# Kernel tuning notes

Hardware: AMD Instinct MI355X
Metric: run time of the kernel (lower is better)

Reference implementation:

```python
import jax, jax.numpy as jnp
import numpy as np

N = 50000
EPS = 1e-16


def _gat_conv(x, w, att_src, att_dst, bias, src, dst, heads, out_ch, concat):
    # x: [N, F_in]; w: [heads*out_ch, F_in]; att_*: [heads, out_ch]; bias: [heads*out_ch] or [out_ch]
    n = x.shape[0]
    xw = (x @ w.T).reshape(n, heads, out_ch)              # [N, H, C]
    a_src = jnp.einsum('nhc,hc->nh', xw, att_src)          # [N, H]
    a_dst = jnp.einsum('nhc,hc->nh', xw, att_dst)
    alpha = a_src[src] + a_dst[dst]                        # [E, H]
    alpha = jax.nn.leaky_relu(alpha, negative_slope=0.2)
    # segment softmax over destination node (every node has a self loop)
    m = jax.ops.segment_max(alpha, dst, num_segments=n)    # [N, H]
    e = jnp.exp(alpha - m[dst])
    s = jax.ops.segment_sum(e, dst, num_segments=n)        # [N, H]
    coef = e / (s[dst] + EPS)                              # [E, H]
    out = jax.ops.segment_sum(xw[src] * coef[:, :, None], dst, num_segments=n)  # [N, H, C]
    if concat:
        out = out.reshape(n, heads * out_ch)
    else:
        out = out.mean(axis=1)
    return out + bias


def setup_inputs() -> dict:
    key = jax.random.key(0)
    ks = jax.random.split(key, 8)
    F_in, H, C1, NC = 128, 2, 64, 16
    E = 1_600_000
    x = jax.random.normal(ks[0], (N, F_in), dtype=jnp.float32)
    edge_index = jax.random.randint(ks[1], (2, E), 0, N, dtype=jnp.int64)
    w1 = jax.random.normal(ks[2], (H * C1, F_in), dtype=jnp.float32) / np.sqrt(F_in)
    att_src1 = jax.random.normal(ks[3], (H, C1), dtype=jnp.float32) / np.sqrt(C1)
    att_dst1 = jax.random.normal(ks[4], (H, C1), dtype=jnp.float32) / np.sqrt(C1)
    b1 = jnp.zeros((H * C1,), dtype=jnp.float32)
    w2 = jax.random.normal(ks[5], (NC, H * C1), dtype=jnp.float32) / np.sqrt(H * C1)
    att_src2 = jax.random.normal(ks[6], (1, NC), dtype=jnp.float32) / np.sqrt(NC)
    att_dst2 = jax.random.normal(ks[7], (1, NC), dtype=jnp.float32) / np.sqrt(NC)
    b2 = jnp.zeros((NC,), dtype=jnp.float32)
    return {"x": x, "edge_index": edge_index, "w1": w1, "att_src1": att_src1,
            "att_dst1": att_dst1, "b1": b1, "w2": w2, "att_src2": att_src2,
            "att_dst2": att_dst2, "b2": b2}


def reference(x, edge_index, w1, att_src1, att_dst1, b1, w2, att_src2, att_dst2, b2):
    n = x.shape[0]
    loop = jnp.arange(n, dtype=edge_index.dtype)
    src = jnp.concatenate([edge_index[0], loop])  # PyG adds self loops by default
    dst = jnp.concatenate([edge_index[1], loop])
    h = _gat_conv(x, w1, att_src1, att_dst1, b1, src, dst, heads=2, out_ch=64, concat=True)
    h = jax.nn.relu(h)
    # dropout p=0.5 is identity in eval mode
    out = _gat_conv(h, w2, att_src2, att_dst2, b2, src, dst, heads=1, out_ch=16, concat=True)
    return out
```

## Files before the change

kernel.cpp:

```cpp
#include <hip/hip_runtime.h>
#include <hip/hip_fp16.h>


#define BSHIFT 7
#define MAXB 512

using f16x8 = __attribute__((ext_vector_type(8))) _Float16;
using f16x4 = __attribute__((ext_vector_type(4))) _Float16;
using f32x4 = __attribute__((ext_vector_type(4))) float;

__device__ __forceinline__ float lrelu(float a) { return fmaxf(a, 0.2f * a); }


__global__ __launch_bounds__(256) void init_cursor_kernel(int* __restrict__ bincur,
                                                          int B, int CAP) {
  int i = blockIdx.x * 256 + threadIdx.x;
  if (i < B) bincur[i] = i * CAP;
}

__global__ __launch_bounds__(256) void partition_kernel(const int* __restrict__ src,
                                                        const int* __restrict__ dst,
                                                        int* __restrict__ bincur,
                                                        unsigned* __restrict__ binned,
                                                        int E, int B, int CH) {
  __shared__ int s_h[MAXB];
  __shared__ int s_base[MAXB];
  __shared__ int s_cur[MAXB];
  for (int i = threadIdx.x; i < B; i += 256) s_h[i] = 0;
  __syncthreads();
  int lo = blockIdx.x * CH, hi = min(lo + CH, E);
  for (int e = lo + threadIdx.x; e < hi; e += 256)
    atomicAdd(&s_h[dst[e] >> BSHIFT], 1);
  __syncthreads();
  for (int i = threadIdx.x; i < B; i += 256) {
    int c = s_h[i];
    s_base[i] = c ? atomicAdd(&bincur[i], c) : 0;
    s_cur[i] = 0;
  }
  __syncthreads();
  for (int e = lo + threadIdx.x; e < hi; e += 256) {
    int d = dst[e];
    int b = d >> BSHIFT;
    int r = atomicAdd(&s_cur[b], 1);
    binned[s_base[b] + r] = (unsigned)src[e] | ((unsigned)(d & 127) << 16);
  }
}

__global__ __launch_bounds__(256) void bucket_build_kernel(const unsigned* __restrict__ binned,
                                                           const int* __restrict__ bincur,
                                                           int2* __restrict__ nodeseg,
                                                           int* __restrict__ csr,
                                                           int N, int CAP) {
  __shared__ int s_deg[128];
  __shared__ int s_cur[128];
  __shared__ int s_wsum;
  int b = blockIdx.x;
  int lo = b * CAP, hi = bincur[b];
  int t = threadIdx.x;
  if (t < 128) s_deg[t] = 0;
  __syncthreads();
  for (int i = lo + t; i < hi; i += 256)
    atomicAdd(&s_deg[binned[i] >> 16], 1);
  __syncthreads();
  int lane = t & 63, wv = t >> 6;
  int v = (t < 128) ? s_deg[t] : 0;
  int incl = v;
#pragma unroll
  for (int off = 1; off < 64; off <<= 1) {
    int u = __shfl_up(incl, off);
    if (lane >= off) incl += u;
  }
  if (t == 63) s_wsum = incl;
  __syncthreads();
  int excl = incl - v + ((wv == 1) ? s_wsum : 0);
  if (t < 128) {
    int node = (b << BSHIFT) + t;
    if (node < N) nodeseg[node] = make_int2(lo + excl, lo + excl + v);
    s_cur[t] = lo + excl;
  }
  __syncthreads();
  for (int i = lo + t; i < hi; i += 256) {
    unsigned e = binned[i];
    int p = atomicAdd(&s_cur[e >> 16], 1);
    csr[p] = (int)(e & 0xFFFFu);
  }
}


#define XS 136
__global__ __launch_bounds__(256) void gemm1_kernel(const float* __restrict__ x,
                                                    const float* __restrict__ w1,
                                                    const float* __restrict__ as1,
                                                    const float* __restrict__ ad1,
                                                    __half* __restrict__ xw1h,
                                                    float* __restrict__ asrc1,
                                                    float* __restrict__ adst1, int N) {
  __shared__ __align__(16) _Float16 lx[64 * XS];
  __shared__ __align__(16) _Float16 lw[128 * XS];
  int t = threadIdx.x;
  int n0 = blockIdx.x * 64;

#pragma unroll
  for (int j = 0; j < 8; ++j) {
    int idx = t + 256 * j;
    int nd = idx >> 5, i4 = (idx & 31) * 4;
    int gn = n0 + nd;
    float4 v = (gn < N) ? *(const float4*)&x[(size_t)gn * 128 + i4]
                        : make_float4(0.f, 0.f, 0.f, 0.f);
    f16x4 h;
    h[0] = (_Float16)v.x; h[1] = (_Float16)v.y;
    h[2] = (_Float16)v.z; h[3] = (_Float16)v.w;
    *(f16x4*)&lx[nd * XS + i4] = h;
  }
#pragma unroll
  for (int j = 0; j < 16; ++j) {
    int idx = t + 256 * j;
    int o = idx >> 5, i4 = (idx & 31) * 4;
    float4 v = *(const float4*)&w1[(size_t)o * 128 + i4];
    f16x4 h;
    h[0] = (_Float16)v.x; h[1] = (_Float16)v.y;
    h[2] = (_Float16)v.z; h[3] = (_Float16)v.w;
    *(f16x4*)&lw[o * XS + i4] = h;
  }
  __syncthreads();

  int lane = t & 63, wv = t >> 6;
  int m16 = lane & 15, q = lane >> 4;

  f32x4 acc[8];
#pragma unroll
  for (int i = 0; i < 8; ++i) acc[i] = (f32x4){0.f, 0.f, 0.f, 0.f};

#pragma unroll
  for (int c = 0; c < 4; ++c) {
    f16x8 a = *(const f16x8*)&lx[(16 * wv + m16) * XS + c * 32 + q * 8];
#pragma unroll
    for (int tt = 0; tt < 8; ++tt) {
      f16x8 b = *(const f16x8*)&lw[(tt * 16 + m16) * XS + c * 32 + q * 8];
      acc[tt] = __builtin_amdgcn_mfma_f32_16x16x32_f16(a, b, acc[tt], 0, 0, 0);
    }
  }

#pragma unroll
  for (int tt = 0; tt < 8; ++tt) {
#pragma unroll
    for (int r = 0; r < 4; ++r) {
      lx[(16 * wv + 4 * q + r) * XS + tt * 16 + m16] = (_Float16)acc[tt][r];
    }
  }

  {
    float ps = 0.f, pd = 0.f;
    int p = q;
#pragma unroll
    for (int k = 0; k < 4; ++k) {
      f16x8 hv = *(const f16x8*)&lx[(16 * wv + m16) * XS + p * 32 + k * 8];
      float4 s0 = *(const float4*)&as1[p * 32 + k * 8];
      float4 s1 = *(const float4*)&as1[p * 32 + k * 8 + 4];
      float4 d0 = *(const float4*)&ad1[p * 32 + k * 8];
      float4 d1 = *(const float4*)&ad1[p * 32 + k * 8 + 4];
      ps += (float)hv[0] * s0.x + (float)hv[1] * s0.y + (float)hv[2] * s0.z +
            (float)hv[3] * s0.w + (float)hv[4] * s1.x + (float)hv[5] * s1.y +
            (float)hv[6] * s1.z + (float)hv[7] * s1.w;
      pd += (float)hv[0] * d0.x + (float)hv[1] * d0.y + (float)hv[2] * d0.z +
            (float)hv[3] * d0.w + (float)hv[4] * d1.x + (float)hv[5] * d1.y +
            (float)hv[6] * d1.z + (float)hv[7] * d1.w;
    }
    ps += __shfl_xor(ps, 16);
    pd += __shfl_xor(pd, 16);
    int n = n0 + 16 * wv + m16;
    if (n < N && (q == 0 || q == 2)) {
      int hh = q >> 1;
      asrc1[2 * n + hh] = ps;
      adst1[2 * n + hh] = pd;
    }
  }

#pragma unroll
  for (int i = 0; i < 4; ++i) {
    int m = q + 4 * i;
    int n = n0 + 16 * wv + m;
    if (n < N) {
      uint4 v = *(const uint4*)&lx[(16 * wv + m) * XS + m16 * 8];
      *(uint4*)&xw1h[(size_t)n * 128 + m16 * 8] = v;
    }
  }
}

__global__ __launch_bounds__(256) void agg1_kernel(const __half* __restrict__ xw1h,
                                                   const float* __restrict__ asrc1,
                                                   const float* __restrict__ adst1,
                                                   const float* __restrict__ b1,
                                                   const float* __restrict__ w2,
                                                   const float* __restrict__ as2,
                                                   const float* __restrict__ ad2,
                                                   const int* __restrict__ csr,
                                                   const int2* __restrict__ nodeseg,
                                                   __half* __restrict__ xw2h,
                                                   float* __restrict__ asrc2,
                                                   float* __restrict__ adst2, int N) {
  __shared__ int s_off[4][64];
  __shared__ float2 s_w[4][64];
  int lane = threadIdx.x & 63, wv = threadIdx.x >> 6;
  int d = blockIdx.x * 4 + wv;
  if (d >= N) return;
  int c8 = lane & 15;
  int row = lane >> 4;
  int head = c8 >> 3;
  int2 seg = nodeseg[d];
  int e0 = seg.x, e1 = seg.y;
  float2 asv = *(const float2*)&asrc1[2 * d];
  float2 adv = *(const float2*)&adst1[2 * d];
  float wself = __expf(lrelu(head ? (asv.y + adv.y) : (asv.x + adv.x)));

  const char* xb = (const char*)xw1h + 16 * c8;

  float a[8];
  float sum = 0.f;
#pragma unroll
  for (int k = 0; k < 8; ++k) a[k] = 0.f;
  if (row == 0) {
    uint4 r = *(const uint4*)(xb + ((size_t)d << 8));
    const __half2* hp = (const __half2*)&r;
#pragma unroll
    for (int k = 0; k < 4; ++k) {
      float2 v = __half22float2(hp[k]);
      a[2 * k] = wself * v.x;
      a[2 * k + 1] = wself * v.y;
    }
    sum = wself;
  }

  for (int base = e0; base < e1; base += 64) {
    int cnt = min(64, e1 - base);
    if (lane < cnt) {
      int s = csr[base + lane];
      float2 aa = *(const float2*)&asrc1[2 * s];
      s_off[wv][lane] = s << 8;
      float2 w;
      w.x = __expf(lrelu(aa.x + adv.x));
      w.y = __expf(lrelu(aa.y + adv.y));
      s_w[wv][lane] = w;
    }
    int j = 0;
    for (; j + 7 < cnt; j += 8) {
      int oA = s_off[wv][j + row];
      int oB = s_off[wv][j + 4 + row];
      float wA = ((const float*)&s_w[wv][j + row])[head];
      float wB = ((const float*)&s_w[wv][j + 4 + row])[head];
      uint4 rA = *(const uint4*)(xb + oA);
      uint4 rB = *(const uint4*)(xb + oB);
      const __half2* hA = (const __half2*)&rA;
      const __half2* hB = (const __half2*)&rB;
#pragma unroll
      for (int k = 0; k < 4; ++k) {
        float2 vA = __half22float2(hA[k]);
        float2 vB = __half22float2(hB[k]);
        a[2 * k] += wA * vA.x + wB * vB.x;
        a[2 * k + 1] += wA * vA.y + wB * vB.y;
      }
      sum += wA + wB;
    }
    for (; j < cnt; j += 4) {
      if (row < cnt - j) {
        int oA = s_off[wv][j + row];
        float wA = ((const float*)&s_w[wv][j + row])[head];
        uint4 rA = *(const uint4*)(xb + oA);
        const __half2* hA = (const __half2*)&rA;
#pragma unroll
        for (int k = 0; k < 4; ++k) {
          float2 vA = __half22float2(hA[k]);
          a[2 * k] += wA * vA.x;
          a[2 * k + 1] += wA * vA.y;
        }
        sum += wA;
      }
    }
  }

#pragma unroll
  for (int k = 0; k < 8; ++k) {
    a[k] += __shfl_xor(a[k], 16);
    a[k] += __shfl_xor(a[k], 32);
  }
  sum += __shfl_xor(sum, 16);
  sum += __shfl_xor(sum, 32);

  float inv = 1.f / (sum + 1e-16f);
  float4 blo = *(const float4*)&b1[8 * c8];
  float4 bhi = *(const float4*)&b1[8 * c8 + 4];
  float h[8];
  h[0] = fmaxf(a[0] * inv + blo.x, 0.f);
  h[1] = fmaxf(a[1] * inv + blo.y, 0.f);
  h[2] = fmaxf(a[2] * inv + blo.z, 0.f);
  h[3] = fmaxf(a[3] * inv + blo.w, 0.f);
  h[4] = fmaxf(a[4] * inv + bhi.x, 0.f);
  h[5] = fmaxf(a[5] * inv + bhi.y, 0.f);
  h[6] = fmaxf(a[6] * inv + bhi.z, 0.f);
  h[7] = fmaxf(a[7] * inv + bhi.w, 0.f);

  float p[4];
#pragma unroll
  for (int cc = 0; cc < 4; ++cc) {
    const float4 wlo = *(const float4*)&w2[(row * 4 + cc) * 128 + 8 * c8];
    const float4 whi = *(const float4*)&w2[(row * 4 + cc) * 128 + 8 * c8 + 4];
    p[cc] = h[0] * wlo.x + h[1] * wlo.y + h[2] * wlo.z + h[3] * wlo.w +
            h[4] * whi.x + h[5] * whi.y + h[6] * whi.z + h[7] * whi.w;
#pragma unroll
    for (int k = 1; k < 16; k <<= 1) p[cc] += __shfl_xor(p[cc], k);
  }
  float qs = 0.f, qd = 0.f;
#pragma unroll
  for (int cc = 0; cc < 4; ++cc) {
    qs += p[cc] * as2[row * 4 + cc];
    qd += p[cc] * ad2[row * 4 + cc];
  }
  qs += __shfl_xor(qs, 16);
  qs += __shfl_xor(qs, 32);
  qd += __shfl_xor(qd, 16);
  qd += __shfl_xor(qd, 32);
  if (lane == 0) {
    asrc2[d] = qs;
    adst2[d] = qd;
  }
  if (c8 == 0) {
    union {
      __half hh[4];
      uint2 u;
    } pk;
#pragma unroll
    for (int cc = 0; cc < 4; ++cc) pk.hh[cc] = __float2half(p[cc]);
    *(uint2*)&xw2h[(size_t)d * 16 + row * 4] = pk.u;
  }
}

__global__ __launch_bounds__(256) void agg2_kernel(const __half* __restrict__ xw2h,
                                                   const float* __restrict__ asrc2,
                                                   const float* __restrict__ adst2,
                                                   const float* __restrict__ b2,
                                                   const int* __restrict__ csr,
                                                   const int2* __restrict__ nodeseg,
                                                   float* __restrict__ out, int N) {
  __shared__ int s_off[4][64];
  __shared__ float s_w[4][64];
  int lane = threadIdx.x & 63, wv = threadIdx.x >> 6;
  int d = blockIdx.x * 4 + wv;
  if (d >= N) return;
  int c2 = lane & 7;
  int row = lane >> 3;
  int2 seg = nodeseg[d];
  int e0 = seg.x, e1 = seg.y;
  float advd = adst2[d];
  float wself = __expf(lrelu(asrc2[d] + advd));
  const char* xb = (const char*)xw2h + 4 * c2;

  float a0 = 0.f, a1 = 0.f, sum = 0.f;
  if (row == 0) {
    float2 v = __half22float2(*(const __half2*)(xb + (size_t)d * 32));
    a0 = wself * v.x;
    a1 = wself * v.y;
    sum = wself;
  }
  for (int base = e0; base < e1; base += 64) {
    int cnt = min(64, e1 - base);
    if (lane < cnt) {
      int s = csr[base + lane];
      s_off[wv][lane] = s << 5;
      s_w[wv][lane] = __expf(lrelu(asrc2[s] + advd));
    }
    int j = 0;
    for (; j + 15 < cnt; j += 16) {
      int o0 = s_off[wv][j + row];
      int o1 = s_off[wv][j + 8 + row];
      float w0 = s_w[wv][j + row];
      float w1 = s_w[wv][j + 8 + row];
      float2 v0 = __half22float2(*(const __half2*)(xb + o0));
      float2 v1 = __half22float2(*(const __half2*)(xb + o1));
      a0 += w0 * v0.x + w1 * v1.x;
      a1 += w0 * v0.y + w1 * v1.y;
      sum += w0 + w1;
    }
    for (; j + 7 < cnt; j += 8) {
      int o0 = s_off[wv][j + row];
      float w0 = s_w[wv][j + row];
      float2 v0 = __half22float2(*(const __half2*)(xb + o0));
      a0 += w0 * v0.x;
      a1 += w0 * v0.y;
      sum += w0;
    }
    if (row < cnt - j) {
      int o0 = s_off[wv][j + row];
      float w0 = s_w[wv][j + row];
      float2 v0 = __half22float2(*(const __half2*)(xb + o0));
      a0 += w0 * v0.x;
      a1 += w0 * v0.y;
      sum += w0;
    }
  }
#pragma unroll
  for (int k = 8; k < 64; k <<= 1) {
    a0 += __shfl_xor(a0, k);
    a1 += __shfl_xor(a1, k);
    sum += __shfl_xor(sum, k);
  }
  if (lane < 8) {
    float inv = 1.f / (sum + 1e-16f);
    float2 r;
    r.x = a0 * inv + b2[2 * c2];
    r.y = a1 * inv + b2[2 * c2 + 1];
    *(float2*)&out[(size_t)d * 16 + 2 * c2] = r;
  }
}


extern "C" void kernel_launch(void* const* d_in, const int* in_sizes, int n_in,
                              void* d_out, int out_size, void* d_ws, size_t ws_size,
                              hipStream_t stream) {
  const float* x = (const float*)d_in[0];
  const int* ei = (const int*)d_in[1];
  const float* w1 = (const float*)d_in[2];
  const float* as1 = (const float*)d_in[3];
  const float* ad1 = (const float*)d_in[4];
  const float* b1 = (const float*)d_in[5];
  const float* w2 = (const float*)d_in[6];
  const float* as2 = (const float*)d_in[7];
  const float* ad2 = (const float*)d_in[8];
  const float* b2 = (const float*)d_in[9];
  float* out = (float*)d_out;

  int N = in_sizes[0] / 128;
  int E = in_sizes[1] / 2;
  const int* srcp = ei;
  const int* dstp = ei + E;

  int B = (N + (1 << BSHIFT) - 1) >> BSHIFT;
  int mean = (E + B - 1) / B;
  int CAP = (mean + mean / 4 + 512 + 255) & ~255;
  const int NB = 256;
  int CH = (E + NB - 1) / NB;

  char* p = (char*)d_ws;
  auto alloc = [&](size_t bytes) -> void* {
    void* r = (void*)p;
    p += (bytes + 255) & ~(size_t)255;
    return r;
  };
  __half* xw1h = (__half*)alloc((size_t)N * 128 * 2);
  float* asrc1 = (float*)alloc((size_t)N * 2 * 4);
  float* adst1 = (float*)alloc((size_t)N * 2 * 4);
  __half* xw2h = (__half*)alloc((size_t)N * 16 * 2);
  float* asrc2 = (float*)alloc((size_t)N * 4);
  float* adst2 = (float*)alloc((size_t)N * 4);
  int2* nodeseg = (int2*)alloc((size_t)N * 8);
  int* csr = (int*)alloc((size_t)B * CAP * 4);
  unsigned* binned = (unsigned*)alloc((size_t)B * CAP * 4);
  int* bincur = (int*)alloc((size_t)B * 4);

  init_cursor_kernel<<<(B + 255) / 256, 256, 0, stream>>>(bincur, B, CAP);
  partition_kernel<<<NB, 256, 0, stream>>>(srcp, dstp, bincur, binned, E, B, CH);
  bucket_build_kernel<<<B, 256, 0, stream>>>(binned, bincur, nodeseg, csr, N, CAP);

  gemm1_kernel<<<(N + 63) / 64, 256, 0, stream>>>(x, w1, as1, ad1, xw1h, asrc1, adst1, N);
  agg1_kernel<<<(N + 3) / 4, 256, 0, stream>>>(xw1h, asrc1, adst1, b1, w2, as2, ad2,
                                               csr, nodeseg, xw2h, asrc2, adst2, N);
  agg2_kernel<<<(N + 3) / 4, 256, 0, stream>>>(xw2h, asrc2, adst2, b2, csr, nodeseg, out, N);
}
```

Measured before the change: 227.4 us.

## Fuse edge partition with GEMM1, stage buckets in LDS, shrink CSR to u16

Merges the edge-partition kernel and the first GEMM into one launch, with block ranges assigned to each role, so the two independent stages run concurrently. The cursor-init kernel is replaced by a memset. Bucket build now stages each bin's edges in shared memory instead of reading global memory twice. CSR indices are stored as 16-bit values to halve index traffic in both aggregation kernels. This relies on N fitting in 16 bits, and the extra shared memory in bucket build may lower occupancy.

Result: no change. 222.9 us (-1.9%).

```diff
diff --git a/kernel.cpp b/kernel.cpp
--- a/kernel.cpp
+++ b/kernel.cpp
@@ -4,6 +4,8 @@
 
 #define BSHIFT 7
 #define MAXB 512
+#define CAPMAX 6144
+#define XS 136
 
 using f16x8 = __attribute__((ext_vector_type(8))) _Float16;
 using f16x4 = __attribute__((ext_vector_type(4))) _Float16;
@@ -12,93 +14,45 @@
 __device__ __forceinline__ float lrelu(float a) { return fmaxf(a, 0.2f * a); }
 
 
-__global__ __launch_bounds__(256) void init_cursor_kernel(int* __restrict__ bincur,
-                                                          int B, int CAP) {
-  int i = blockIdx.x * 256 + threadIdx.x;
-  if (i < B) bincur[i] = i * CAP;
-}
-
-__global__ __launch_bounds__(256) void partition_kernel(const int* __restrict__ src,
-                                                        const int* __restrict__ dst,
-                                                        int* __restrict__ bincur,
-                                                        unsigned* __restrict__ binned,
-                                                        int E, int B, int CH) {
-  __shared__ int s_h[MAXB];
-  __shared__ int s_base[MAXB];
-  __shared__ int s_cur[MAXB];
-  for (int i = threadIdx.x; i < B; i += 256) s_h[i] = 0;
-  __syncthreads();
-  int lo = blockIdx.x * CH, hi = min(lo + CH, E);
-  for (int e = lo + threadIdx.x; e < hi; e += 256)
-    atomicAdd(&s_h[dst[e] >> BSHIFT], 1);
-  __syncthreads();
-  for (int i = threadIdx.x; i < B; i += 256) {
-    int c = s_h[i];
-    s_base[i] = c ? atomicAdd(&bincur[i], c) : 0;
-    s_cur[i] = 0;
-  }
-  __syncthreads();
-  for (int e = lo + threadIdx.x; e < hi; e += 256) {
-    int d = dst[e];
-    int b = d >> BSHIFT;
-    int r = atomicAdd(&s_cur[b], 1);
-    binned[s_base[b] + r] = (unsigned)src[e] | ((unsigned)(d & 127) << 16);
-  }
-}
-
-__global__ __launch_bounds__(256) void bucket_build_kernel(const unsigned* __restrict__ binned,
-                                                           const int* __restrict__ bincur,
-                                                           int2* __restrict__ nodeseg,
-                                                           int* __restrict__ csr,
-                                                           int N, int CAP) {
-  __shared__ int s_deg[128];
-  __shared__ int s_cur[128];
-  __shared__ int s_wsum;
-  int b = blockIdx.x;
-  int lo = b * CAP, hi = bincur[b];
+__global__ __launch_bounds__(256) void part_gemm1_kernel(
+    const int* __restrict__ src, const int* __restrict__ dst,
+    int* __restrict__ bincur, unsigned* __restrict__ binned,
+    int E, int B, int CH, int CAP, int NB,
+    const float* __restrict__ x, const float* __restrict__ w1,
+    const float* __restrict__ as1, const float* __restrict__ ad1,
+    __half* __restrict__ xw1h, float* __restrict__ asrc1,
+    float* __restrict__ adst1, int N) {
+  __shared__ __align__(16) char smem[(64 + 128) * XS * 2];
   int t = threadIdx.x;
-  if (t < 128) s_deg[t] = 0;
-  __syncthreads();
-  for (int i = lo + t; i < hi; i += 256)
-    atomicAdd(&s_deg[binned[i] >> 16], 1);
-  __syncthreads();
-  int lane = t & 63, wv = t >> 6;
-  int v = (t < 128) ? s_deg[t] : 0;
-  int incl = v;
-#pragma unroll
-  for (int off = 1; off < 64; off <<= 1) {
-    int u = __shfl_up(incl, off);
-    if (lane >= off) incl += u;
-  }
-  if (t == 63) s_wsum = incl;
-  __syncthreads();
-  int excl = incl - v + ((wv == 1) ? s_wsum : 0);
-  if (t < 128) {
-    int node = (b << BSHIFT) + t;
-    if (node < N) nodeseg[node] = make_int2(lo + excl, lo + excl + v);
-    s_cur[t] = lo + excl;
-  }
-  __syncthreads();
-  for (int i = lo + t; i < hi; i += 256) {
-    unsigned e = binned[i];
-    int p = atomicAdd(&s_cur[e >> 16], 1);
-    csr[p] = (int)(e & 0xFFFFu);
-  }
-}
-
-
-#define XS 136
-__global__ __launch_bounds__(256) void gemm1_kernel(const float* __restrict__ x,
-                                                    const float* __restrict__ w1,
-                                                    const float* __restrict__ as1,
-                                                    const float* __restrict__ ad1,
-                                                    __half* __restrict__ xw1h,
-                                                    float* __restrict__ asrc1,
-                                                    float* __restrict__ adst1, int N) {
-  __shared__ __align__(16) _Float16 lx[64 * XS];
-  __shared__ __align__(16) _Float16 lw[128 * XS];
-  int t = threadIdx.x;
-  int n0 = blockIdx.x * 64;
+
+  if (blockIdx.x < (unsigned)NB) {
+    int* s_h = (int*)smem;
+    int* s_base = s_h + MAXB;
+    int* s_cur = s_base + MAXB;
+    for (int i = t; i < B; i += 256) s_h[i] = 0;
+    __syncthreads();
+    int lo = blockIdx.x * CH, hi = min(lo + CH, E);
+    for (int e = lo + t; e < hi; e += 256)
+      atomicAdd(&s_h[dst[e] >> BSHIFT], 1);
+    __syncthreads();
+    for (int i = t; i < B; i += 256) {
+      int c = s_h[i];
+      s_base[i] = c ? (i * CAP + atomicAdd(&bincur[i], c)) : 0;
+      s_cur[i] = 0;
+    }
+    __syncthreads();
+    for (int e = lo + t; e < hi; e += 256) {
+      int d = dst[e];
+      int b = d >> BSHIFT;
+      int r = atomicAdd(&s_cur[b], 1);
+      binned[s_base[b] + r] = (unsigned)src[e] | ((unsigned)(d & 127) << 16);
+    }
+    return;
+  }
+
+  _Float16* lx = (_Float16*)smem;
+  _Float16* lw = lx + 64 * XS;
+  int n0 = (blockIdx.x - NB) * 64;
 
 #pragma unroll
   for (int j = 0; j < 8; ++j) {
@@ -187,6 +141,54 @@
   }
 }
 
+
+__global__ __launch_bounds__(256) void bucket_build_kernel(const unsigned* __restrict__ binned,
+                                                           const int* __restrict__ bincur,
+                                                           int2* __restrict__ nodeseg,
+                                                           unsigned short* __restrict__ csr,
+                                                           int N, int CAP) {
+  __shared__ int s_deg[128];
+  __shared__ int s_cur[128];
+  __shared__ int s_wsum;
+  __shared__ unsigned s_edges[CAPMAX];
+  int b = blockIdx.x;
+  int lo = b * CAP, hi = lo + bincur[b];
+  int cnt = hi - lo;
+  int t = threadIdx.x;
+  if (t < 128) s_deg[t] = 0;
+  int stg = min(cnt, CAPMAX);
+  for (int i = t; i < stg; i += 256) s_edges[i] = binned[lo + i];
+  __syncthreads();
+  for (int i = t; i < cnt; i += 256) {
+    unsigned e = (i < CAPMAX) ? s_edges[i] : binned[lo + i];
+    atomicAdd(&s_deg[e >> 16], 1);
+  }
+  __syncthreads();
+  int lane = t & 63, wv = t >> 6;
+  int v = (t < 128) ? s_deg[t] : 0;
+  int incl = v;
+#pragma unroll
+  for (int off = 1; off < 64; off <<= 1) {
+    int u = __shfl_up(incl, off);
+    if (lane >= off) incl += u;
+  }
+  if (t == 63) s_wsum = incl;
+  __syncthreads();
+  int excl = incl - v + ((wv == 1) ? s_wsum : 0);
+  if (t < 128) {
+    int node = (b << BSHIFT) + t;
+    if (node < N) nodeseg[node] = make_int2(lo + excl, lo + excl + v);
+    s_cur[t] = lo + excl;
+  }
+  __syncthreads();
+  for (int i = t; i < cnt; i += 256) {
+    unsigned e = (i < CAPMAX) ? s_edges[i] : binned[lo + i];
+    int p = atomicAdd(&s_cur[e >> 16], 1);
+    csr[p] = (unsigned short)(e & 0xFFFFu);
+  }
+}
+
+
 __global__ __launch_bounds__(256) void agg1_kernel(const __half* __restrict__ xw1h,
                                                    const float* __restrict__ asrc1,
                                                    const float* __restrict__ adst1,
@@ -194,7 +196,7 @@
                                                    const float* __restrict__ w2,
                                                    const float* __restrict__ as2,
                                                    const float* __restrict__ ad2,
-                                                   const int* __restrict__ csr,
+                                                   const unsigned short* __restrict__ csr,
                                                    const int2* __restrict__ nodeseg,
                                                    __half* __restrict__ xw2h,
                                                    float* __restrict__ asrc2,
@@ -234,7 +236,7 @@
   for (int base = e0; base < e1; base += 64) {
     int cnt = min(64, e1 - base);
     if (lane < cnt) {
-      int s = csr[base + lane];
+      int s = (int)csr[base + lane];
       float2 aa = *(const float2*)&asrc1[2 * s];
       s_off[wv][lane] = s << 8;
       float2 w;
@@ -334,11 +336,12 @@
   }
 }
 
+
 __global__ __launch_bounds__(256) void agg2_kernel(const __half* __restrict__ xw2h,
                                                    const float* __restrict__ asrc2,
                                                    const float* __restrict__ adst2,
                                                    const float* __restrict__ b2,
-                                                   const int* __restrict__ csr,
+                                                   const unsigned short* __restrict__ csr,
                                                    const int2* __restrict__ nodeseg,
                                                    float* __restrict__ out, int N) {
   __shared__ int s_off[4][64];
@@ -364,7 +367,7 @@
   for (int base = e0; base < e1; base += 64) {
     int cnt = min(64, e1 - base);
     if (lane < cnt) {
-      int s = csr[base + lane];
+      int s = (int)csr[base + lane];
       s_off[wv][lane] = s << 5;
       s_w[wv][lane] = __expf(lrelu(asrc2[s] + advd));
     }
@@ -438,6 +441,7 @@
   int CAP = (mean + mean / 4 + 512 + 255) & ~255;
   const int NB = 256;
   int CH = (E + NB - 1) / NB;
+  int GB = (N + 63) / 64;
 
   char* p = (char*)d_ws;
   auto alloc = [&](size_t bytes) -> void* {
@@ -452,15 +456,15 @@
   float* asrc2 = (float*)alloc((size_t)N * 4);
   float* adst2 = (float*)alloc((size_t)N * 4);
   int2* nodeseg = (int2*)alloc((size_t)N * 8);
-  int* csr = (int*)alloc((size_t)B * CAP * 4);
+  unsigned short* csr = (unsigned short*)alloc((size_t)B * CAP * 2);
   unsigned* binned = (unsigned*)alloc((size_t)B * CAP * 4);
   int* bincur = (int*)alloc((size_t)B * 4);
 
-  init_cursor_kernel<<<(B + 255) / 256, 256, 0, stream>>>(bincur, B, CAP);
-  partition_kernel<<<NB, 256, 0, stream>>>(srcp, dstp, bincur, binned, E, B, CH);
+  hipMemsetAsync(bincur, 0, (size_t)B * 4, stream);
+  part_gemm1_kernel<<<NB + GB, 256, 0, stream>>>(srcp, dstp, bincur, binned,
+                                                 E, B, CH, CAP, NB,
+                                                 x, w1, as1, ad1, xw1h, asrc1, adst1, N);
   bucket_build_kernel<<<B, 256, 0, stream>>>(binned, bincur, nodeseg, csr, N, CAP);
-
-  gemm1_kernel<<<(N + 63) / 64, 256, 0, stream>>>(x, w1, as1, ad1, xw1h, asrc1, adst1, N);
   agg1_kernel<<<(N + 3) / 4, 256, 0, stream>>>(xw1h, asrc1, adst1, b1, w2, as2, ad2,
                                                csr, nodeseg, xw2h, asrc2, adst2, N);
   agg2_kernel<<<(N + 3) / 4, 256, 0, stream>>>(xw2h, asrc2, adst2, b2, csr, nodeseg, out, N);
```
